# Optimization experiments

Hardware: AMD Instinct MI355X
Metric: run time of the kernel (lower is better)

Reference implementation:

```python
import jax, jax.numpy as jnp
import numpy as np

V, E, H, O, B, T = 50000, 128, 128, 128, 64, 512


def setup_inputs() -> dict:
    key = jax.random.key(0)
    ks = jax.random.split(key, 16)
    s = 0.05
    X = jax.random.randint(ks[0], (B, T), 0, V)
    lens = jnp.sort(jax.random.randint(ks[1], (B,), 64, T + 1))[::-1]
    lens = lens.at[0].set(T)  # pack_padded needs descending lengths, max == T
    emb = jax.random.normal(ks[2], (V, E)) * s
    emb = emb.at[0].set(0.0)  # padding_idx = 0
    return {
        "X": X,
        "X_lengths": lens,
        "batch_size": B,
        "emb": emb,
        "W_e2i": jax.random.normal(ks[3], (H, E)) * s,
        "b_e2i": jax.random.normal(ks[4], (H,)) * s,
        "Wih_f": jax.random.normal(ks[5], (3 * H, H)) * s,
        "Whh_f": jax.random.normal(ks[6], (3 * H, H)) * s,
        "bih_f": jax.random.normal(ks[7], (3 * H,)) * s,
        "bhh_f": jax.random.normal(ks[8], (3 * H,)) * s,
        "Wih_b": jax.random.normal(ks[9], (3 * H, H)) * s,
        "Whh_b": jax.random.normal(ks[10], (3 * H, H)) * s,
        "bih_b": jax.random.normal(ks[11], (3 * H,)) * s,
        "bhh_b": jax.random.normal(ks[12], (3 * H,)) * s,
        "W_h2o": jax.random.normal(ks[13], (O, 2 * H)) * s,
        "b_h2o": jax.random.normal(ks[14], (O,)) * s,
        "u_w": jax.random.uniform(ks[15], (O,)),  # torch.rand
    }


def _gru_scan(gx, mask_tb, Whh, bhh):
    """gx: [T,B,3H] precomputed input gates; mask_tb: [T,B,1] valid-step mask.
    Masked update emulates pack_padded_sequence: padded steps keep h unchanged
    (and h stays 0 before the first valid step of the reversed direction)."""
    h0 = jnp.zeros((gx.shape[1], Whh.shape[1]), gx.dtype)

    def step(h, tb):
        gxt, m = tb
        gh = h @ Whh.T + bhh
        gxr, gxz, gxn = jnp.split(gxt, 3, axis=-1)
        ghr, ghz, ghn = jnp.split(gh, 3, axis=-1)
        r = jax.nn.sigmoid(gxr + ghr)
        z = jax.nn.sigmoid(gxz + ghz)
        n = jnp.tanh(gxn + r * ghn)
        h_new = (1.0 - z) * n + z * h
        h = jnp.where(m, h_new, h)
        return h, h

    _, hs = jax.lax.scan(step, h0, (gx, mask_tb))
    return hs  # [T,B,H]


def reference(X, X_lengths, batch_size, emb, W_e2i, b_e2i,
              Wih_f, Whh_f, bih_f, bhh_f, Wih_b, Whh_b, bih_b, bhh_b,
              W_h2o, b_h2o, u_w):
    x = emb[X]                              # [B,T,E]
    x = x @ W_e2i.T + b_e2i                 # [B,T,H]
    Tn = x.shape[1]
    mask = jnp.arange(Tn)[None, :] < X_lengths[:, None]  # [B,T]
    m_tb = mask.T[:, :, None]               # [T,B,1]

    gx_f = (x @ Wih_f.T + bih_f).transpose(1, 0, 2)       # [T,B,3H]
    h_f = _gru_scan(gx_f, m_tb, Whh_f, bhh_f)             # [T,B,H]
    gx_b = (x @ Wih_b.T + bih_b).transpose(1, 0, 2)[::-1]
    h_b = _gru_scan(gx_b, m_tb[::-1], Whh_b, bhh_b)[::-1]

    Hout = jnp.concatenate([h_f, h_b], axis=-1).transpose(1, 0, 2)  # [B,T,2H]
    Hout = Hout * mask[:, :, None].astype(Hout.dtype)  # pad_packed zeros pads

    Y = jnp.tanh(Hout @ W_h2o.T + b_h2o)               # [B,T,O]
    scores = jnp.where(mask, (Y * u_w).sum(-1), -jnp.inf)  # [B,T]
    alpha = jax.nn.softmax(scores, axis=1)             # per-sample softmax over valid steps
    pooled = jnp.einsum("bt,btd->bd", alpha, Hout)     # [B,2H]
    return pooled[None]                                # [1,B,2H]
```

## Files before the change

### kernel.cpp

```cpp
#include <hip/hip_runtime.h>
#include <hip/hip_bf16.h>

#define VV 50000
#define EE 128
#define HH 128
#define OO 128
#define BB 64
#define TT 512

typedef __bf16 bf16_t;
typedef __attribute__((ext_vector_type(8))) __bf16 bf16x8;
typedef __attribute__((ext_vector_type(4))) __bf16 bf16x4;
typedef __attribute__((ext_vector_type(4))) float floatx4;

#define SC_RZ (-1.4426950408889634f)
#define SC_N  (2.8853900817779268f)

__device__ __forceinline__ bf16x8 ldb8(const bf16_t* p) {
    return *reinterpret_cast<const bf16x8*>(p);
}

__device__ __forceinline__ bf16x8 ldf8_bf(const float* p) {
    const float4* q = reinterpret_cast<const float4*>(p);
    float4 u = q[0], v = q[1];
    bf16x8 r;
    r[0] = (__bf16)u.x; r[1] = (__bf16)u.y; r[2] = (__bf16)u.z; r[3] = (__bf16)u.w;
    r[4] = (__bf16)v.x; r[5] = (__bf16)v.y; r[6] = (__bf16)v.z; r[7] = (__bf16)v.w;
    return r;
}

__device__ __forceinline__ float fast_rcp(float x) { return __builtin_amdgcn_rcpf(x); }
__device__ __forceinline__ float exp2_f(float x) { return __builtin_amdgcn_exp2f(x); }
__device__ __forceinline__ float tanh_f(float x) {
    float e = __expf(2.0f * x);
    return 1.0f - 2.0f * fast_rcp(e + 1.0f);
}

__device__ __forceinline__ void lds_barrier() {
    asm volatile("s_waitcnt lgkmcnt(0)\n\ts_barrier" ::: "memory");
}

__global__ __launch_bounds__(256) void k0_conv(
    const float* __restrict__ we,
    const float* __restrict__ wihf, const float* __restrict__ wihb,
    const float* __restrict__ whhf, const float* __restrict__ whhb,
    const float* __restrict__ wh2o,
    const float* __restrict__ bihf, const float* __restrict__ bhhf,
    const float* __restrict__ bihb, const float* __restrict__ bhhb,
    bf16_t* __restrict__ we_bf,
    bf16_t* __restrict__ wih_bf, bf16_t* __restrict__ whh_bf,
    bf16_t* __restrict__ wh2o_bf, float* __restrict__ gxbias) {
    int tid = blockIdx.x * 256 + threadIdx.x;
    int np = gridDim.x * 256;
    for (int i = tid; i < HH * EE; i += np) we_bf[i] = (bf16_t)we[i];
    for (int i = tid; i < 384 * HH; i += np) {
        int nrow = i >> 7;
        float sc = (nrow < 256) ? SC_RZ : SC_N;
        wih_bf[i] = (bf16_t)(sc * wihf[i]);
        wih_bf[384 * HH + i] = (bf16_t)(sc * wihb[i]);
        whh_bf[i] = (bf16_t)(sc * whhf[i]);
        whh_bf[384 * HH + i] = (bf16_t)(sc * whhb[i]);
    }
    for (int i = tid; i < OO * 256; i += np) wh2o_bf[i] = (bf16_t)wh2o[i];
    if (tid < 768) {
        int dir = tid / 384, n = tid % 384;
        const float* bih = dir ? bihb : bihf;
        const float* bhh = dir ? bhhb : bhhf;
        float sc = (n < 256) ? SC_RZ : SC_N;
        gxbias[tid] = sc * bih[n] + (n < 256 ? sc * bhh[n] : 0.0f);
    }
}

__global__ __launch_bounds__(256) void k12_gx(const int* __restrict__ X,
                                              const float* __restrict__ emb,
                                              const bf16_t* __restrict__ we_bf,
                                              const float* __restrict__ be,
                                              const bf16_t* __restrict__ wih_bf,
                                              const float* __restrict__ gxbias,
                                              const int* __restrict__ lens,
                                              bf16_t* __restrict__ gx3,
                                              unsigned int* __restrict__ ctr) {
    if (blockIdx.x == 0 && threadIdx.x == 0) *ctr = 0u;

    int blk = blockIdx.x;
    int tq = blk >> 2;
    int g = blk & 3;
    if (4 * tq >= lens[16 * g]) return;

    int lane = threadIdx.x & 63;
    int w2 = threadIdx.x >> 6;
    int quad = lane >> 4, col = lane & 15;

    __shared__ bf16_t xs[4][16 * 136];

    {
        int t = 4 * tq + w2;
        int v = X[(g * 16 + col) * TT + t];
        bf16x8 a[4];
#pragma unroll
        for (int kc = 0; kc < 4; ++kc)
            a[kc] = ldf8_bf(emb + (size_t)v * EE + kc * 32 + quad * 8);
#pragma unroll
        for (int nt = 0; nt < 8; ++nt) {
            int n = nt * 16 + col;
            floatx4 acc = {0.f, 0.f, 0.f, 0.f};
#pragma unroll
            for (int kc = 0; kc < 4; ++kc) {
                bf16x8 bw = ldb8(we_bf + (size_t)n * EE + kc * 32 + quad * 8);
                acc = __builtin_amdgcn_mfma_f32_16x16x32_bf16(a[kc], bw, acc, 0, 0, 0);
            }
            float bias = be[n];
#pragma unroll
            for (int r = 0; r < 4; ++r)
                xs[w2][(quad * 4 + r) * 136 + n] = (bf16_t)(acc[r] + bias);
        }
    }
    __syncthreads();

    bf16x8 a2[4][4];
#pragma unroll
    for (int tt = 0; tt < 4; ++tt)
#pragma unroll
        for (int kc = 0; kc < 4; ++kc)
            a2[tt][kc] = ldb8(xs[tt] + col * 136 + kc * 32 + quad * 8);

#pragma unroll 2
    for (int tl = 0; tl < 12; ++tl) {
        int idx = w2 * 12 + tl;
        int dir = idx >= 24;
        int n = (idx - dir * 24) * 16 + col;
        bf16x8 bw[4];
#pragma unroll
        for (int kc = 0; kc < 4; ++kc)
            bw[kc] = ldb8(wih_bf + ((size_t)dir * 384 + n) * HH + kc * 32 + quad * 8);
        float bias = gxbias[dir * 384 + n];
#pragma unroll
        for (int tt = 0; tt < 4; ++tt) {
            int t = 4 * tq + tt;
            floatx4 acc = {0.f, 0.f, 0.f, 0.f};
#pragma unroll
            for (int kc = 0; kc < 4; ++kc)
                acc = __builtin_amdgcn_mfma_f32_16x16x32_bf16(a2[tt][kc], bw[kc], acc, 0, 0, 0);
            bf16x4 pack;
#pragma unroll
            for (int r = 0; r < 4; ++r)
                pack[r] = (__bf16)(acc[r] + bias);
            *reinterpret_cast<bf16x4*>(
                gx3 + (((size_t)(dir * 16 + 4 * g + quad) * TT + t) * 384 + n) * 4) = pack;
        }
    }
}

#define HPAD 144
#define HBUF (4 * HPAD)
__global__ __launch_bounds__(512) void k345(const bf16_t* __restrict__ gx3,
                                            const bf16_t* __restrict__ whh_bf,
                                            const float* __restrict__ bhh_f,
                                            const float* __restrict__ bhh_b,
                                            const int* __restrict__ lens,
                                            const bf16_t* __restrict__ wh2o_bf,
                                            const float* __restrict__ bh2o,
                                            const float* __restrict__ uw,
                                            bf16_t* __restrict__ hist2,
                                            float* __restrict__ out,
                                            unsigned int* __restrict__ ctr) {
    int b = blockIdx.x;
    int tid = threadIdx.x;
    int lane = tid & 63;
    int wv = tid >> 6;
    int quad = lane >> 4, col = lane & 15;

    __shared__ bf16_t hl[2 * HBUF];
    __shared__ float smax[TT][4];
    __shared__ float alpha[TT];
    __shared__ float redw[16];
    __shared__ float red2[16 * 32 * 9];

    if (b < 32) {
        int g16 = b & 15;
        int dir = b >> 4;
        const float* bhh = dir ? bhh_b : bhh_f;
        int j = 16 * wv + col;

        for (int i = tid; i < 2 * HBUF; i += 512) hl[i] = (bf16_t)0.f;

        int len1 = lens[4 * g16 + quad];
        int Lmax = max(max(lens[4 * g16], lens[4 * g16 + 1]),
                       max(lens[4 * g16 + 2], lens[4 * g16 + 3]));

        float bhn = SC_N * bhh[256 + j];

        bf16x8 Bw[3][4];
#pragma unroll
        for (int gate = 0; gate < 3; ++gate)
#pragma unroll
            for (int kc = 0; kc < 4; ++kc)
                Bw[gate][kc] = ldb8(whh_bf + ((size_t)dir * 384 + gate * 128 + j) * HH + kc * 32 + quad * 8);

        const bf16_t* gbase = gx3 + (size_t)(dir * 16 + g16) * TT * 1536;
        bf16_t* hb = hist2 + (size_t)(dir * 16 + g16) * TT * 512;
        int loff[3];
#pragma unroll
        for (int gate = 0; gate < 3; ++gate)
            loff[gate] = (gate * 128 + j) * 4 + quad;
        int hoff = quad * 128 + j;
        int aoff = (col >> 2) * HPAD + quad * 8;

        float h = 0.f;
        int S4 = (Lmax + 3) & ~3;

        __bf16 ring[4][3];
#pragma unroll
        for (int u = 0; u < 4; ++u) {
            int t = dir ? (Lmax - 1 - u) : u;
#pragma unroll
            for (int gate = 0; gate < 3; ++gate)
                ring[u][gate] = gbase[(size_t)t * 1536 + loff[gate]];
        }
        lds_barrier();

        int gstep = dir ? -1536 : 1536;
        int hstep = dir ? -512 : 512;
        const bf16_t* rp0 = gbase + (size_t)(dir ? (Lmax - 5) : 4) * 1536 + loff[0];
        const bf16_t* rp1 = gbase + (size_t)(dir ? (Lmax - 5) : 4) * 1536 + loff[1];
        const bf16_t* rp2 = gbase + (size_t)(dir ? (Lmax - 5) : 4) * 1536 + loff[2];
        bf16_t* hp = hb + (size_t)(dir ? (Lmax - 1) : 0) * 512 + hoff;
        int ulo = dir ? (Lmax - len1) : 0;
        int uhi = dir ? Lmax : len1;

        for (int sb = 0; sb < S4; sb += 4) {
#pragma unroll
            for (int u = 0; u < 4; ++u) {
                int s = sb + u;
                const bf16_t* hc = hl + (s & 1) * HBUF;
                bf16_t* hn = hl + ((s + 1) & 1) * HBUF;

                float gx0 = (float)ring[u][0];
                float gx1 = (float)ring[u][1];
                float gx2 = (float)ring[u][2];

                bf16x8 a[4];
#pragma unroll
                for (int kc = 0; kc < 4; ++kc)
                    a[kc] = ldb8(hc + aoff + kc * 32);

                floatx4 cr = {0.f, 0.f, 0.f, 0.f};
                floatx4 cz = {0.f, 0.f, 0.f, 0.f};
                floatx4 cn = {bhn, bhn, bhn, bhn};
#pragma unroll
                for (int kc = 0; kc < 4; ++kc) {
                    cr = __builtin_amdgcn_mfma_f32_16x16x32_bf16(a[kc], Bw[0][kc], cr, 0, 0, 0);
                    cz = __builtin_amdgcn_mfma_f32_16x16x32_bf16(a[kc], Bw[1][kc], cz, 0, 0, 0);
                    cn = __builtin_amdgcn_mfma_f32_16x16x32_bf16(a[kc], Bw[2][kc], cn, 0, 0, 0);
                }

                ring[u][0] = *rp0;
                ring[u][1] = *rp1;
                ring[u][2] = *rp2;
                {
                    int adv = (s < Lmax - 5) ? gstep : 0;
                    rp0 += adv; rp1 += adv; rp2 += adv;
                }

                float rg = fast_rcp(1.0f + exp2_f(cr[0] + gx0));
                float zg = fast_rcp(1.0f + exp2_f(cz[0] + gx1));
                float v  = fmaf(rg, cn[0], gx2);
                float ng = fmaf(-2.0f, fast_rcp(exp2_f(v) + 1.0f), 1.0f);
                float hnew = fmaf(zg, h - ng, ng);

                bool upd = (s >= ulo) && (s < uhi);
                h = upd ? hnew : h;
                bf16_t h16 = (bf16_t)h;
                hn[quad * HPAD + j] = h16;
                *hp = h16;
                hp += (s < Lmax - 1) ? hstep : 0;

                lds_barrier();
            }
        }

        __threadfence();
        __syncthreads();
        if (tid == 0)
            __hip_atomic_fetch_add(ctr, 1u, __ATOMIC_RELEASE, __HIP_MEMORY_SCOPE_AGENT);
    }

    if (tid == 0) {
        while (__hip_atomic_load(ctr, __ATOMIC_ACQUIRE, __HIP_MEMORY_SCOPE_AGENT) < 32u)
            __builtin_amdgcn_s_sleep(8);
    }
    __syncthreads();
    __threadfence();

    {
        int g16 = b >> 2, bl = b & 3;
        int len = lens[b];
        int p = wv >> 2;
        int q = wv & 3;

        const bf16_t* hf = hist2 + (size_t)g16 * TT * 512 + bl * 128;
        const bf16_t* hbk = hist2 + (size_t)(16 + g16) * TT * 512 + bl * 128;

        int n0 = (q * 2 + 0) * 16 + col;
        int n1 = (q * 2 + 1) * 16 + col;
        float bias0 = bh2o[n0], u0 = uw[n0];
        float bias1 = bh2o[n1], u1 = uw[n1];

        bf16x8 bw0[8], bw1[8];
#pragma unroll
        for (int kc = 0; kc < 8; ++kc) {
            bw0[kc] = ldb8(wh2o_bf + (size_t)n0 * 256 + kc * 32 + quad * 8);
            bw1[kc] = ldb8(wh2o_bf + (size_t)n1 * 256 + kc * 32 + quad * 8);
        }

        int nch = (len + 15) >> 4;
        bf16x8 a[8], an[8];
        {
            int t = p * 16 + col;
#pragma unroll
            for (int kc = 0; kc < 4; ++kc) {
                a[kc]     = ldb8(hf  + (size_t)t * 512 + kc * 32 + quad * 8);
                a[kc + 4] = ldb8(hbk + (size_t)t * 512 + kc * 32 + quad * 8);
            }
        }
        for (int ch = p; ch < nch; ch += 2) {
            int t0 = ch * 16;
            {
                int tn = (ch + 2 < nch ? t0 + 32 : t0) + col;
#pragma unroll
                for (int kc = 0; kc < 4; ++kc) {
                    an[kc]     = ldb8(hf  + (size_t)tn * 512 + kc * 32 + quad * 8);
                    an[kc + 4] = ldb8(hbk + (size_t)tn * 512 + kc * 32 + quad * 8);
                }
            }
            float p4[4] = {0.f, 0.f, 0.f, 0.f};
#pragma unroll
            for (int tl = 0; tl < 2; ++tl) {
                float bias = tl ? bias1 : bias0;
                float u = tl ? u1 : u0;
                floatx4 accA = {0.f, 0.f, 0.f, 0.f};
                floatx4 accB = {0.f, 0.f, 0.f, 0.f};
#pragma unroll
                for (int kc = 0; kc < 4; ++kc) {
                    bf16x8 bwA = tl ? bw1[kc] : bw0[kc];
                    bf16x8 bwB = tl ? bw1[kc + 4] : bw0[kc + 4];
                    accA = __builtin_amdgcn_mfma_f32_16x16x32_bf16(a[kc], bwA, accA, 0, 0, 0);
                    accB = __builtin_amdgcn_mfma_f32_16x16x32_bf16(a[kc + 4], bwB, accB, 0, 0, 0);
                }
#pragma unroll
                for (int r = 0; r < 4; ++r)
                    p4[r] += tanh_f(accA[r] + accB[r] + bias) * u;
            }
#pragma unroll
            for (int m = 1; m < 16; m <<= 1)
#pragma unroll
                for (int r = 0; r < 4; ++r)
                    p4[r] += __shfl_xor(p4[r], m, 64);
            if (col == 0) {
#pragma unroll
                for (int r = 0; r < 4; ++r)
                    smax[t0 + quad * 4 + r][q] = p4[r];
            }
#pragma unroll
            for (int kc = 0; kc < 8; ++kc) a[kc] = an[kc];
        }
        __syncthreads();

        int t = tid;
        float s = -1e30f;
        if (t < len) s = smax[t][0] + smax[t][1] + smax[t][2] + smax[t][3];
        float m = s;
#pragma unroll
        for (int off = 1; off <= 32; off <<= 1) m = fmaxf(m, __shfl_xor(m, off, 64));
        if (lane == 0) redw[wv] = m;
        __syncthreads();
        float mx = fmaxf(fmaxf(fmaxf(redw[0], redw[1]), fmaxf(redw[2], redw[3])),
                         fmaxf(fmaxf(redw[4], redw[5]), fmaxf(redw[6], redw[7])));
        float e = (t < len) ? __expf(s - mx) : 0.f;
        alpha[t] = e;
        float sm = e;
#pragma unroll
        for (int off = 1; off <= 32; off <<= 1) sm += __shfl_xor(sm, off, 64);
        if (lane == 0) redw[8 + wv] = sm;
        __syncthreads();
        float inv = fast_rcp(redw[8] + redw[9] + redw[10] + redw[11] +
                             redw[12] + redw[13] + redw[14] + redw[15]);

        {
            int ts = tid >> 5, o = tid & 31;
            int dirp = o >> 4;
            int j8 = (o & 15) * 8;
            const bf16_t* hbase = (dirp ? hbk : hf) + j8;
            float acc8[8];
#pragma unroll
            for (int ee = 0; ee < 8; ++ee) acc8[ee] = 0.f;
            for (int tt2 = ts; tt2 < len; tt2 += 16) {
                float al = alpha[tt2];
                bf16x8 hv = ldb8(hbase + (size_t)tt2 * 512);
#pragma unroll
                for (int ee = 0; ee < 8; ++ee) acc8[ee] = fmaf(al, (float)hv[ee], acc8[ee]);
            }
#pragma unroll
            for (int ee = 0; ee < 8; ++ee) red2[(ts * 32 + o) * 9 + ee] = acc8[ee];
            __syncthreads();
            if (tid < 256) {
                int c = tid;
                int dir2 = c >> 7, rem = c & 127;
                int oo = dir2 * 16 + (rem >> 3), ee = c & 7;
                float acc = 0.f;
#pragma unroll
                for (int qq = 0; qq < 16; ++qq) acc += red2[(qq * 32 + oo) * 9 + ee];
                out[(size_t)b * 256 + c] = acc * inv;
            }
        }
    }
}

extern "C" void kernel_launch(void* const* d_in, const int* in_sizes, int n_in,
                              void* d_out, int out_size, void* d_ws, size_t ws_size,
                              hipStream_t stream) {
    const int* X       = (const int*)d_in[0];
    const int* lens    = (const int*)d_in[1];
    const float* emb   = (const float*)d_in[3];
    const float* We2i  = (const float*)d_in[4];
    const float* be2i  = (const float*)d_in[5];
    const float* Wihf  = (const float*)d_in[6];
    const float* Whhf  = (const float*)d_in[7];
    const float* bihf  = (const float*)d_in[8];
    const float* bhhf  = (const float*)d_in[9];
    const float* Wihb  = (const float*)d_in[10];
    const float* Whhb  = (const float*)d_in[11];
    const float* bihb  = (const float*)d_in[12];
    const float* bhhb  = (const float*)d_in[13];
    const float* Wh2o  = (const float*)d_in[14];
    const float* bh2o  = (const float*)d_in[15];
    const float* uw    = (const float*)d_in[16];

    char* ws = (char*)d_ws;
    size_t off = 0;
    bf16_t* we_bf = (bf16_t*)(ws + off);   off += (size_t)HH * EE * 2;
    bf16_t* wih_bf = (bf16_t*)(ws + off);  off += (size_t)2 * 384 * HH * 2;
    bf16_t* whh_bf = (bf16_t*)(ws + off);  off += (size_t)2 * 384 * HH * 2;
    bf16_t* wh2o_bf = (bf16_t*)(ws + off); off += (size_t)OO * 256 * 2;
    float* gxbias = (float*)(ws + off);    off += 768 * 4;
    off = (off + 255) & ~(size_t)255;
    unsigned int* ctr = (unsigned int*)(ws + off); off += 256;
    bf16_t* gx3 = (bf16_t*)(ws + off);     off += (size_t)32 * TT * 384 * 4 * 2;
    bf16_t* hist2 = (bf16_t*)(ws + off);   off += (size_t)32 * TT * 4 * 128 * 2;

    float* out = (float*)d_out;

    k0_conv<<<dim3(256), dim3(256), 0, stream>>>(We2i, Wihf, Wihb, Whhf, Whhb,
                                                 Wh2o, bihf, bhhf, bihb, bhhb,
                                                 we_bf, wih_bf, whh_bf, wh2o_bf, gxbias);
    k12_gx<<<dim3(TT), dim3(256), 0, stream>>>(X, emb, we_bf, be2i, wih_bf, gxbias, lens, gx3, ctr);
    k345<<<dim3(BB), dim3(512), 0, stream>>>(gx3, whh_bf, bhhf, bhhb, lens,
                                             wh2o_bf, bh2o, uw, hist2, out, ctr);
}
```

Before: 373.0 us.

## Split fused GRU+pool kernel into two launches, dropping atomic grid barrier

The fused kernel ran 32 GRU blocks and then made all 64 blocks spin on a global atomic counter before the attention pooling stage. This splits it into a GRU kernel (16x2 grid) and a separate pooling kernel ordered by the stream, which removes the counter, the spin-wait and the threadfences. It also lets each kernel use only its own shared memory, which could help occupancy. The cost is one extra kernel launch, and pooling can no longer start while other blocks are still in the GRU.

```diff
diff --git a/kernel.cpp b/kernel.cpp
--- a/kernel.cpp
+++ b/kernel.cpp
@@ -78,10 +78,7 @@
                                               const bf16_t* __restrict__ wih_bf,
                                               const float* __restrict__ gxbias,
                                               const int* __restrict__ lens,
-                                              bf16_t* __restrict__ gx3,
-                                              unsigned int* __restrict__ ctr) {
-    if (blockIdx.x == 0 && threadIdx.x == 0) *ctr = 0u;
-
+                                              bf16_t* __restrict__ gx3) {
     int blk = blockIdx.x;
     int tq = blk >> 2;
     int g = blk & 3;
@@ -153,265 +150,255 @@
 
 #define HPAD 144
 #define HBUF (4 * HPAD)
-__global__ __launch_bounds__(512) void k345(const bf16_t* __restrict__ gx3,
-                                            const bf16_t* __restrict__ whh_bf,
-                                            const float* __restrict__ bhh_f,
-                                            const float* __restrict__ bhh_b,
-                                            const int* __restrict__ lens,
-                                            const bf16_t* __restrict__ wh2o_bf,
-                                            const float* __restrict__ bh2o,
-                                            const float* __restrict__ uw,
-                                            bf16_t* __restrict__ hist2,
-                                            float* __restrict__ out,
-                                            unsigned int* __restrict__ ctr) {
+__global__ __launch_bounds__(512) void k3_gru(const bf16_t* __restrict__ gx3,
+                                              const bf16_t* __restrict__ whh_bf,
+                                              const float* __restrict__ bhh_f,
+                                              const float* __restrict__ bhh_b,
+                                              const int* __restrict__ lens,
+                                              bf16_t* __restrict__ hist2) {
+    int g16 = blockIdx.x;
+    int dir = blockIdx.y;
+    const float* bhh = dir ? bhh_b : bhh_f;
+
+    int tid = threadIdx.x;
+    int w = tid >> 6;
+    int lane = tid & 63;
+    int quad = lane >> 4, col = lane & 15;
+    int j = 16 * w + col;
+
+    __shared__ bf16_t hl[2 * HBUF];
+    for (int i = tid; i < 2 * HBUF; i += 512) hl[i] = (bf16_t)0.f;
+
+    int len1 = lens[4 * g16 + quad];
+    int Lmax = max(max(lens[4 * g16], lens[4 * g16 + 1]),
+                   max(lens[4 * g16 + 2], lens[4 * g16 + 3]));
+
+    float bhn = SC_N * bhh[256 + j];
+
+    bf16x8 Bw[3][4];
+#pragma unroll
+    for (int gate = 0; gate < 3; ++gate)
+#pragma unroll
+        for (int kc = 0; kc < 4; ++kc)
+            Bw[gate][kc] = ldb8(whh_bf + ((size_t)dir * 384 + gate * 128 + j) * HH + kc * 32 + quad * 8);
+
+    const bf16_t* gbase = gx3 + (size_t)(dir * 16 + g16) * TT * 1536;
+    bf16_t* hb = hist2 + (size_t)(dir * 16 + g16) * TT * 512;
+    int loff[3];
+#pragma unroll
+    for (int gate = 0; gate < 3; ++gate)
+        loff[gate] = (gate * 128 + j) * 4 + quad;
+    int hoff = quad * 128 + j;
+    int aoff = (col >> 2) * HPAD + quad * 8;
+
+    float h = 0.f;
+    int S4 = (Lmax + 3) & ~3;
+
+    __bf16 ring[4][3];
+#pragma unroll
+    for (int u = 0; u < 4; ++u) {
+        int t = dir ? (Lmax - 1 - u) : u;
+#pragma unroll
+        for (int gate = 0; gate < 3; ++gate)
+            ring[u][gate] = gbase[(size_t)t * 1536 + loff[gate]];
+    }
+    lds_barrier();
+
+    int gstep = dir ? -1536 : 1536;
+    int hstep = dir ? -512 : 512;
+    const bf16_t* rp0 = gbase + (size_t)(dir ? (Lmax - 5) : 4) * 1536 + loff[0];
+    const bf16_t* rp1 = gbase + (size_t)(dir ? (Lmax - 5) : 4) * 1536 + loff[1];
+    const bf16_t* rp2 = gbase + (size_t)(dir ? (Lmax - 5) : 4) * 1536 + loff[2];
+    bf16_t* hp = hb + (size_t)(dir ? (Lmax - 1) : 0) * 512 + hoff;
+    int ulo = dir ? (Lmax - len1) : 0;
+    int uhi = dir ? Lmax : len1;
+
+    for (int sb = 0; sb < S4; sb += 4) {
+#pragma unroll
+        for (int u = 0; u < 4; ++u) {
+            int s = sb + u;
+            const bf16_t* hc = hl + (s & 1) * HBUF;
+            bf16_t* hn = hl + ((s + 1) & 1) * HBUF;
+
+            float gx0 = (float)ring[u][0];
+            float gx1 = (float)ring[u][1];
+            float gx2 = (float)ring[u][2];
+
+            bf16x8 a[4];
+#pragma unroll
+            for (int kc = 0; kc < 4; ++kc)
+                a[kc] = ldb8(hc + aoff + kc * 32);
+
+            floatx4 cr = {0.f, 0.f, 0.f, 0.f};
+            floatx4 cz = {0.f, 0.f, 0.f, 0.f};
+            floatx4 cn = {bhn, bhn, bhn, bhn};
+#pragma unroll
+            for (int kc = 0; kc < 4; ++kc) {
+                cr = __builtin_amdgcn_mfma_f32_16x16x32_bf16(a[kc], Bw[0][kc], cr, 0, 0, 0);
+                cz = __builtin_amdgcn_mfma_f32_16x16x32_bf16(a[kc], Bw[1][kc], cz, 0, 0, 0);
+                cn = __builtin_amdgcn_mfma_f32_16x16x32_bf16(a[kc], Bw[2][kc], cn, 0, 0, 0);
+            }
+
+            ring[u][0] = *rp0;
+            ring[u][1] = *rp1;
+            ring[u][2] = *rp2;
+            {
+                int adv = (s < Lmax - 5) ? gstep : 0;
+                rp0 += adv; rp1 += adv; rp2 += adv;
+            }
+
+            float rg = fast_rcp(1.0f + exp2_f(cr[0] + gx0));
+            float zg = fast_rcp(1.0f + exp2_f(cz[0] + gx1));
+            float v  = fmaf(rg, cn[0], gx2);
+            float ng = fmaf(-2.0f, fast_rcp(exp2_f(v) + 1.0f), 1.0f);
+            float hnew = fmaf(zg, h - ng, ng);
+
+            bool upd = (s >= ulo) && (s < uhi);
+            h = upd ? hnew : h;
+            bf16_t h16 = (bf16_t)h;
+            hn[quad * HPAD + j] = h16;
+            *hp = h16;
+            hp += (s < Lmax - 1) ? hstep : 0;
+
+            lds_barrier();
+        }
+    }
+}
+
+__global__ __launch_bounds__(512) void k45_pool(const bf16_t* __restrict__ hist2,
+                                                const bf16_t* __restrict__ wh2o_bf,
+                                                const float* __restrict__ bh2o,
+                                                const float* __restrict__ uw,
+                                                const int* __restrict__ lens,
+                                                float* __restrict__ out) {
     int b = blockIdx.x;
+    int g16 = b >> 2, bl = b & 3;
     int tid = threadIdx.x;
-    int lane = tid & 63;
-    int wv = tid >> 6;
+    int lane = tid & 63, wv = tid >> 6;
     int quad = lane >> 4, col = lane & 15;
-
-    __shared__ bf16_t hl[2 * HBUF];
+    int len = lens[b];
+
+    int p = wv >> 2;
+    int q = wv & 3;
+
     __shared__ float smax[TT][4];
     __shared__ float alpha[TT];
     __shared__ float redw[16];
     __shared__ float red2[16 * 32 * 9];
 
-    if (b < 32) {
-        int g16 = b & 15;
-        int dir = b >> 4;
-        const float* bhh = dir ? bhh_b : bhh_f;
-        int j = 16 * wv + col;
-
-        for (int i = tid; i < 2 * HBUF; i += 512) hl[i] = (bf16_t)0.f;
-
-        int len1 = lens[4 * g16 + quad];
-        int Lmax = max(max(lens[4 * g16], lens[4 * g16 + 1]),
-                       max(lens[4 * g16 + 2], lens[4 * g16 + 3]));
-
-        float bhn = SC_N * bhh[256 + j];
-
-        bf16x8 Bw[3][4];
-#pragma unroll
-        for (int gate = 0; gate < 3; ++gate)
-#pragma unroll
-            for (int kc = 0; kc < 4; ++kc)
-                Bw[gate][kc] = ldb8(whh_bf + ((size_t)dir * 384 + gate * 128 + j) * HH + kc * 32 + quad * 8);
-
-        const bf16_t* gbase = gx3 + (size_t)(dir * 16 + g16) * TT * 1536;
-        bf16_t* hb = hist2 + (size_t)(dir * 16 + g16) * TT * 512;
-        int loff[3];
-#pragma unroll
-        for (int gate = 0; gate < 3; ++gate)
-            loff[gate] = (gate * 128 + j) * 4 + quad;
-        int hoff = quad * 128 + j;
-        int aoff = (col >> 2) * HPAD + quad * 8;
-
-        float h = 0.f;
-        int S4 = (Lmax + 3) & ~3;
-
-        __bf16 ring[4][3];
-#pragma unroll
-        for (int u = 0; u < 4; ++u) {
-            int t = dir ? (Lmax - 1 - u) : u;
-#pragma unroll
-            for (int gate = 0; gate < 3; ++gate)
-                ring[u][gate] = gbase[(size_t)t * 1536 + loff[gate]];
-        }
-        lds_barrier();
-
-        int gstep = dir ? -1536 : 1536;
-        int hstep = dir ? -512 : 512;
-        const bf16_t* rp0 = gbase + (size_t)(dir ? (Lmax - 5) : 4) * 1536 + loff[0];
-        const bf16_t* rp1 = gbase + (size_t)(dir ? (Lmax - 5) : 4) * 1536 + loff[1];
-        const bf16_t* rp2 = gbase + (size_t)(dir ? (Lmax - 5) : 4) * 1536 + loff[2];
-        bf16_t* hp = hb + (size_t)(dir ? (Lmax - 1) : 0) * 512 + hoff;
-        int ulo = dir ? (Lmax - len1) : 0;
-        int uhi = dir ? Lmax : len1;
-
-        for (int sb = 0; sb < S4; sb += 4) {
-#pragma unroll
-            for (int u = 0; u < 4; ++u) {
-                int s = sb + u;
-                const bf16_t* hc = hl + (s & 1) * HBUF;
-                bf16_t* hn = hl + ((s + 1) & 1) * HBUF;
-
-                float gx0 = (float)ring[u][0];
-                float gx1 = (float)ring[u][1];
-                float gx2 = (float)ring[u][2];
-
-                bf16x8 a[4];
-#pragma unroll
-                for (int kc = 0; kc < 4; ++kc)
-                    a[kc] = ldb8(hc + aoff + kc * 32);
-
-                floatx4 cr = {0.f, 0.f, 0.f, 0.f};
-                floatx4 cz = {0.f, 0.f, 0.f, 0.f};
-                floatx4 cn = {bhn, bhn, bhn, bhn};
-#pragma unroll
-                for (int kc = 0; kc < 4; ++kc) {
-                    cr = __builtin_amdgcn_mfma_f32_16x16x32_bf16(a[kc], Bw[0][kc], cr, 0, 0, 0);
-                    cz = __builtin_amdgcn_mfma_f32_16x16x32_bf16(a[kc], Bw[1][kc], cz, 0, 0, 0);
-                    cn = __builtin_amdgcn_mfma_f32_16x16x32_bf16(a[kc], Bw[2][kc], cn, 0, 0, 0);
-                }
-
-                ring[u][0] = *rp0;
-                ring[u][1] = *rp1;
-                ring[u][2] = *rp2;
-                {
-                    int adv = (s < Lmax - 5) ? gstep : 0;
-                    rp0 += adv; rp1 += adv; rp2 += adv;
-                }
-
-                float rg = fast_rcp(1.0f + exp2_f(cr[0] + gx0));
-                float zg = fast_rcp(1.0f + exp2_f(cz[0] + gx1));
-                float v  = fmaf(rg, cn[0], gx2);
-                float ng = fmaf(-2.0f, fast_rcp(exp2_f(v) + 1.0f), 1.0f);
-                float hnew = fmaf(zg, h - ng, ng);
-
-                bool upd = (s >= ulo) && (s < uhi);
-                h = upd ? hnew : h;
-                bf16_t h16 = (bf16_t)h;
-                hn[quad * HPAD + j] = h16;
-                *hp = h16;
-                hp += (s < Lmax - 1) ? hstep : 0;
-
-                lds_barrier();
+    const bf16_t* hf = hist2 + (size_t)g16 * TT * 512 + bl * 128;
+    const bf16_t* hbk = hist2 + (size_t)(16 + g16) * TT * 512 + bl * 128;
+
+    int n0 = (q * 2 + 0) * 16 + col;
+    int n1 = (q * 2 + 1) * 16 + col;
+    float bias0 = bh2o[n0], u0 = uw[n0];
+    float bias1 = bh2o[n1], u1 = uw[n1];
+
+    bf16x8 bw0[8], bw1[8];
+#pragma unroll
+    for (int kc = 0; kc < 8; ++kc) {
+        bw0[kc] = ldb8(wh2o_bf + (size_t)n0 * 256 + kc * 32 + quad * 8);
+        bw1[kc] = ldb8(wh2o_bf + (size_t)n1 * 256 + kc * 32 + quad * 8);
+    }
+
+    int nch = (len + 15) >> 4;
+    bf16x8 a[8], an[8];
+    {
+        int t = p * 16 + col;
+#pragma unroll
+        for (int kc = 0; kc < 4; ++kc) {
+            a[kc]     = ldb8(hf  + (size_t)t * 512 + kc * 32 + quad * 8);
+            a[kc + 4] = ldb8(hbk + (size_t)t * 512 + kc * 32 + quad * 8);
+        }
+    }
+    for (int ch = p; ch < nch; ch += 2) {
+        int t0 = ch * 16;
+        {
+            int tn = (ch + 2 < nch ? t0 + 32 : t0) + col;
+#pragma unroll
+            for (int kc = 0; kc < 4; ++kc) {
+                an[kc]     = ldb8(hf  + (size_t)tn * 512 + kc * 32 + quad * 8);
+                an[kc + 4] = ldb8(hbk + (size_t)tn * 512 + kc * 32 + quad * 8);
             }
         }
-
-        __threadfence();
+        float p4[4] = {0.f, 0.f, 0.f, 0.f};
+#pragma unroll
+        for (int tl = 0; tl < 2; ++tl) {
+            float bias = tl ? bias1 : bias0;
+            float u = tl ? u1 : u0;
+            floatx4 accA = {0.f, 0.f, 0.f, 0.f};
+            floatx4 accB = {0.f, 0.f, 0.f, 0.f};
+#pragma unroll
+            for (int kc = 0; kc < 4; ++kc) {
+                bf16x8 bwA = tl ? bw1[kc] : bw0[kc];
+                bf16x8 bwB = tl ? bw1[kc + 4] : bw0[kc + 4];
+                accA = __builtin_amdgcn_mfma_f32_16x16x32_bf16(a[kc], bwA, accA, 0, 0, 0);
+                accB = __builtin_amdgcn_mfma_f32_16x16x32_bf16(a[kc + 4], bwB, accB, 0, 0, 0);
+            }
+#pragma unroll
+            for (int r = 0; r < 4; ++r)
+                p4[r] += tanh_f(accA[r] + accB[r] + bias) * u;
+        }
+#pragma unroll
+        for (int m = 1; m < 16; m <<= 1)
+#pragma unroll
+            for (int r = 0; r < 4; ++r)
+                p4[r] += __shfl_xor(p4[r], m, 64);
+        if (col == 0) {
+#pragma unroll
+            for (int r = 0; r < 4; ++r)
+                smax[t0 + quad * 4 + r][q] = p4[r];
+        }
+#pragma unroll
+        for (int kc = 0; kc < 8; ++kc) a[kc] = an[kc];
+    }
+    __syncthreads();
+
+    int t = tid;
+    float s = -1e30f;
+    if (t < len) s = smax[t][0] + smax[t][1] + smax[t][2] + smax[t][3];
+    float m = s;
+#pragma unroll
+    for (int off = 1; off <= 32; off <<= 1) m = fmaxf(m, __shfl_xor(m, off, 64));
+    if (lane == 0) redw[wv] = m;
+    __syncthreads();
+    float mx = fmaxf(fmaxf(fmaxf(redw[0], redw[1]), fmaxf(redw[2], redw[3])),
+                     fmaxf(fmaxf(redw[4], redw[5]), fmaxf(redw[6], redw[7])));
+    float e = (t < len) ? __expf(s - mx) : 0.f;
+    alpha[t] = e;
+    float sm = e;
+#pragma unroll
+    for (int off = 1; off <= 32; off <<= 1) sm += __shfl_xor(sm, off, 64);
+    if (lane == 0) redw[8 + wv] = sm;
+    __syncthreads();
+    float inv = fast_rcp(redw[8] + redw[9] + redw[10] + redw[11] +
+                         redw[12] + redw[13] + redw[14] + redw[15]);
+
+    {
+        int ts = tid >> 5, o = tid & 31;
+        int dirp = o >> 4;
+        int j8 = (o & 15) * 8;
+        const bf16_t* hbase = (dirp ? hbk : hf) + j8;
+        float acc8[8];
+#pragma unroll
+        for (int ee = 0; ee < 8; ++ee) acc8[ee] = 0.f;
+        for (int tt2 = ts; tt2 < len; tt2 += 16) {
+            float al = alpha[tt2];
+            bf16x8 hv = ldb8(hbase + (size_t)tt2 * 512);
+#pragma unroll
+            for (int ee = 0; ee < 8; ++ee) acc8[ee] = fmaf(al, (float)hv[ee], acc8[ee]);
+        }
+#pragma unroll
+        for (int ee = 0; ee < 8; ++ee) red2[(ts * 32 + o) * 9 + ee] = acc8[ee];
         __syncthreads();
-        if (tid == 0)
-            __hip_atomic_fetch_add(ctr, 1u, __ATOMIC_RELEASE, __HIP_MEMORY_SCOPE_AGENT);
-    }
-
-    if (tid == 0) {
-        while (__hip_atomic_load(ctr, __ATOMIC_ACQUIRE, __HIP_MEMORY_SCOPE_AGENT) < 32u)
-            __builtin_amdgcn_s_sleep(8);
-    }
-    __syncthreads();
-    __threadfence();
-
-    {
-        int g16 = b >> 2, bl = b & 3;
-        int len = lens[b];
-        int p = wv >> 2;
-        int q = wv & 3;
-
-        const bf16_t* hf = hist2 + (size_t)g16 * TT * 512 + bl * 128;
-        const bf16_t* hbk = hist2 + (size_t)(16 + g16) * TT * 512 + bl * 128;
-
-        int n0 = (q * 2 + 0) * 16 + col;
-        int n1 = (q * 2 + 1) * 16 + col;
-        float bias0 = bh2o[n0], u0 = uw[n0];
-        float bias1 = bh2o[n1], u1 = uw[n1];
-
-        bf16x8 bw0[8], bw1[8];
-#pragma unroll
-        for (int kc = 0; kc < 8; ++kc) {
-            bw0[kc] = ldb8(wh2o_bf + (size_t)n0 * 256 + kc * 32 + quad * 8);
-            bw1[kc] = ldb8(wh2o_bf + (size_t)n1 * 256 + kc * 32 + quad * 8);
-        }
-
-        int nch = (len + 15) >> 4;
-        bf16x8 a[8], an[8];
-        {
-            int t = p * 16 + col;
-#pragma unroll
-            for (int kc = 0; kc < 4; ++kc) {
-                a[kc]     = ldb8(hf  + (size_t)t * 512 + kc * 32 + quad * 8);
-                a[kc + 4] = ldb8(hbk + (size_t)t * 512 + kc * 32 + quad * 8);
-            }
-        }
-        for (int ch = p; ch < nch; ch += 2) {
-            int t0 = ch * 16;
-            {
-                int tn = (ch + 2 < nch ? t0 + 32 : t0) + col;
-#pragma unroll
-                for (int kc = 0; kc < 4; ++kc) {
-                    an[kc]     = ldb8(hf  + (size_t)tn * 512 + kc * 32 + quad * 8);
-                    an[kc + 4] = ldb8(hbk + (size_t)tn * 512 + kc * 32 + quad * 8);
-                }
-            }
-            float p4[4] = {0.f, 0.f, 0.f, 0.f};
-#pragma unroll
-            for (int tl = 0; tl < 2; ++tl) {
-                float bias = tl ? bias1 : bias0;
-                float u = tl ? u1 : u0;
-                floatx4 accA = {0.f, 0.f, 0.f, 0.f};
-                floatx4 accB = {0.f, 0.f, 0.f, 0.f};
-#pragma unroll
-                for (int kc = 0; kc < 4; ++kc) {
-                    bf16x8 bwA = tl ? bw1[kc] : bw0[kc];
-                    bf16x8 bwB = tl ? bw1[kc + 4] : bw0[kc + 4];
-                    accA = __builtin_amdgcn_mfma_f32_16x16x32_bf16(a[kc], bwA, accA, 0, 0, 0);
-                    accB = __builtin_amdgcn_mfma_f32_16x16x32_bf16(a[kc + 4], bwB, accB, 0, 0, 0);
-                }
-#pragma unroll
-                for (int r = 0; r < 4; ++r)
-                    p4[r] += tanh_f(accA[r] + accB[r] + bias) * u;
-            }
-#pragma unroll
-            for (int m = 1; m < 16; m <<= 1)
-#pragma unroll
-                for (int r = 0; r < 4; ++r)
-                    p4[r] += __shfl_xor(p4[r], m, 64);
-            if (col == 0) {
-#pragma unroll
-                for (int r = 0; r < 4; ++r)
-                    smax[t0 + quad * 4 + r][q] = p4[r];
-            }
-#pragma unroll
-            for (int kc = 0; kc < 8; ++kc) a[kc] = an[kc];
-        }
-        __syncthreads();
-
-        int t = tid;
-        float s = -1e30f;
-        if (t < len) s = smax[t][0] + smax[t][1] + smax[t][2] + smax[t][3];
-        float m = s;
-#pragma unroll
-        for (int off = 1; off <= 32; off <<= 1) m = fmaxf(m, __shfl_xor(m, off, 64));
-        if (lane == 0) redw[wv] = m;
-        __syncthreads();
-        float mx = fmaxf(fmaxf(fmaxf(redw[0], redw[1]), fmaxf(redw[2], redw[3])),
-                         fmaxf(fmaxf(redw[4], redw[5]), fmaxf(redw[6], redw[7])));
-        float e = (t < len) ? __expf(s - mx) : 0.f;
-        alpha[t] = e;
-        float sm = e;
-#pragma unroll
-        for (int off = 1; off <= 32; off <<= 1) sm += __shfl_xor(sm, off, 64);
-        if (lane == 0) redw[8 + wv] = sm;
-        __syncthreads();
-        float inv = fast_rcp(redw[8] + redw[9] + redw[10] + redw[11] +
-                             redw[12] + redw[13] + redw[14] + redw[15]);
-
-        {
-            int ts = tid >> 5, o = tid & 31;
-            int dirp = o >> 4;
-            int j8 = (o & 15) * 8;
-            const bf16_t* hbase = (dirp ? hbk : hf) + j8;
-            float acc8[8];
-#pragma unroll
-            for (int ee = 0; ee < 8; ++ee) acc8[ee] = 0.f;
-            for (int tt2 = ts; tt2 < len; tt2 += 16) {
-                float al = alpha[tt2];
-                bf16x8 hv = ldb8(hbase + (size_t)tt2 * 512);
-#pragma unroll
-                for (int ee = 0; ee < 8; ++ee) acc8[ee] = fmaf(al, (float)hv[ee], acc8[ee]);
-            }
-#pragma unroll
-            for (int ee = 0; ee < 8; ++ee) red2[(ts * 32 + o) * 9 + ee] = acc8[ee];
-            __syncthreads();
-            if (tid < 256) {
-                int c = tid;
-                int dir2 = c >> 7, rem = c & 127;
-                int oo = dir2 * 16 + (rem >> 3), ee = c & 7;
-                float acc = 0.f;
-#pragma unroll
-                for (int qq = 0; qq < 16; ++qq) acc += red2[(qq * 32 + oo) * 9 + ee];
-                out[(size_t)b * 256 + c] = acc * inv;
-            }
+        if (tid < 256) {
+            int c = tid;
+            int dir2 = c >> 7, rem = c & 127;
+            int oo = dir2 * 16 + (rem >> 3), ee = c & 7;
+            float acc = 0.f;
+#pragma unroll
+            for (int qq = 0; qq < 16; ++qq) acc += red2[(qq * 32 + oo) * 9 + ee];
+            out[(size_t)b * 256 + c] = acc * inv;
         }
     }
 }
@@ -444,7 +431,6 @@
     bf16_t* wh2o_bf = (bf16_t*)(ws + off); off += (size_t)OO * 256 * 2;
     float* gxbias = (float*)(ws + off);    off += 768 * 4;
     off = (off + 255) & ~(size_t)255;
-    unsigned int* ctr = (unsigned int*)(ws + off); off += 256;
     bf16_t* gx3 = (bf16_t*)(ws + off);     off += (size_t)32 * TT * 384 * 4 * 2;
     bf16_t* hist2 = (bf16_t*)(ws + off);   off += (size_t)32 * TT * 4 * 128 * 2;
 
@@ -453,7 +439,7 @@
     k0_conv<<<dim3(256), dim3(256), 0, stream>>>(We2i, Wihf, Wihb, Whhf, Whhb,
                                                  Wh2o, bihf, bhhf, bihb, bhhb,
                                                  we_bf, wih_bf, whh_bf, wh2o_bf, gxbias);
-    k12_gx<<<dim3(TT), dim3(256), 0, stream>>>(X, emb, we_bf, be2i, wih_bf, gxbias, lens, gx3, ctr);
-    k345<<<dim3(BB), dim3(512), 0, stream>>>(gx3, whh_bf, bhhf, bhhb, lens,
-                                             wh2o_bf, bh2o, uw, hist2, out, ctr);
-}
+    k12_gx<<<dim3(TT), dim3(256), 0, stream>>>(X, emb, we_bf, be2i, wih_bf, gxbias, lens, gx3);
+    k3_gru<<<dim3(16, 2), dim3(512), 0, stream>>>(gx3, whh_bf, bhhf, bhhb, lens, hist2);
+    k45_pool<<<dim3(BB), dim3(512), 0, stream>>>(hist2, wh2o_bf, bh2o, uw, lens, out);
+}
```

New measurement: 341.7 us. 8.4% less time.
